# Kernel tuning notes

Measured on AMD Instinct MI355X. Metric: run time of the kernel, lower is better.

The kernel has to match this reference:

```python
import jax, jax.numpy as jnp
import numpy as np

EMBED_DIM = 512
NUM_HEADS = 8
HEAD_DIM = EMBED_DIM // NUM_HEADS


def setup_inputs() -> dict:
    key = jax.random.key(0)
    ks = jax.random.split(key, 9)
    s = 1.0 / np.sqrt(EMBED_DIM)
    x = jax.random.normal(ks[0], (2, 4096, EMBED_DIM), dtype=jnp.float32)
    return {
        "x": x,
        "Wq": jax.random.uniform(ks[1], (EMBED_DIM, EMBED_DIM), jnp.float32, -s, s),
        "bq": jax.random.uniform(ks[2], (EMBED_DIM,), jnp.float32, -s, s),
        "Wk": jax.random.uniform(ks[3], (EMBED_DIM, EMBED_DIM), jnp.float32, -s, s),
        "bk": jax.random.uniform(ks[4], (EMBED_DIM,), jnp.float32, -s, s),
        "Wv": jax.random.uniform(ks[5], (EMBED_DIM, EMBED_DIM), jnp.float32, -s, s),
        "bv": jax.random.uniform(ks[6], (EMBED_DIM,), jnp.float32, -s, s),
        "Wo": jax.random.uniform(ks[7], (EMBED_DIM, EMBED_DIM), jnp.float32, -s, s),
        "bo": jax.random.uniform(ks[8], (EMBED_DIM,), jnp.float32, -s, s),
    }


def reference(x, Wq, bq, Wk, bk, Wv, bv, Wo, bo):
    B, S, E = x.shape
    H, D = NUM_HEADS, HEAD_DIM
    # projections (torch Linear: x @ W.T + b)
    q = (x @ Wq.T + bq).reshape(B, S, H, D).transpose(0, 2, 1, 3)  # [B,H,S,D]
    k = (x @ Wk.T + bk).reshape(B, S, H, D).transpose(0, 2, 1, 3)
    v = (x @ Wv.T + bv).reshape(B, S, H, D).transpose(0, 2, 1, 3)
    scores = jnp.einsum("bhsd,bhtd->bhst", q, k) / np.sqrt(D)  # [B,H,S,S]
    attn = jax.nn.softmax(scores, axis=-1)
    out = jnp.einsum("bhst,bhtd->bhsd", attn, v)  # [B,H,S,D]
    out = out.transpose(0, 2, 1, 3).reshape(B, S, E)
    return out @ Wo.T + bo + x
```

## Files before the change

kernel.cpp:

```cpp
#include <hip/hip_runtime.h>
#include <hip/hip_bf16.h>


typedef __attribute__((ext_vector_type(8))) short short8;
typedef __attribute__((ext_vector_type(4))) float floatx4;

#define SEQ 4096
#define EMB 512
#define NH 8
#define HD 64
#define MROWS 8192
#define SC2 0.18033688011112042f

__device__ inline unsigned short f2bf_rne(float f) {
    union { float f; unsigned int u; } c; c.f = f;
    unsigned int u = c.u;
    return (unsigned short)((u + 0x7FFFu + ((u >> 16) & 1u)) >> 16);
}

__device__ inline short8 load8f(const float* __restrict__ p) {
    float4 a = *(const float4*)p;
    float4 b = *(const float4*)(p + 4);
    short8 r;
    r[0] = (short)f2bf_rne(a.x); r[1] = (short)f2bf_rne(a.y);
    r[2] = (short)f2bf_rne(a.z); r[3] = (short)f2bf_rne(a.w);
    r[4] = (short)f2bf_rne(b.x); r[5] = (short)f2bf_rne(b.y);
    r[6] = (short)f2bf_rne(b.z); r[7] = (short)f2bf_rne(b.w);
    return r;
}

__device__ inline void gload_lds16(const unsigned short* g, unsigned short* l) {
    __builtin_amdgcn_global_load_lds(
        (__attribute__((address_space(1))) void*)(void*)g,
        (__attribute__((address_space(3))) void*)l,
        16, 0, 0);
}

__global__ __launch_bounds__(256) void convert_kernel(
    const float* __restrict__ x, const float* __restrict__ Wq,
    const float* __restrict__ Wk, const float* __restrict__ Wv,
    const float* __restrict__ Wo, unsigned short* __restrict__ xb,
    unsigned short* __restrict__ wb)
{
    const size_t i8 = ((size_t)blockIdx.x * 256 + threadIdx.x) * 8;
    const float* src; unsigned short* dst;
    if (i8 < (size_t)MROWS * EMB) { src = x + i8; dst = xb + i8; }
    else {
        size_t j = i8 - (size_t)MROWS * EMB;
        int w = (int)(j >> 18); size_t off = j & 262143;
        src = (w == 0 ? Wq : w == 1 ? Wk : w == 2 ? Wv : Wo) + off;
        dst = wb + (size_t)w * 262144 + off;
    }
    *(short8*)dst = load8f(src);
}

__global__ __launch_bounds__(256) void qkv_kernel(
    const unsigned short* __restrict__ xb, const unsigned short* __restrict__ wb,
    const float* __restrict__ bq, const float* __restrict__ bk,
    const float* __restrict__ bv, unsigned short* __restrict__ Qo,
    unsigned short* __restrict__ Ko, unsigned short* __restrict__ VTo)
{
    __shared__ unsigned short sA[2][8192];
    __shared__ unsigned short sB[2][8192];

    const int tid = threadIdx.x, wave = tid >> 6, lane = tid & 63;
    const int quad = lane >> 4, l16 = lane & 15;
    const int wm = wave >> 1, wn = wave & 1;
    const int row0 = blockIdx.x * 128, col0 = blockIdx.y * 128;
    const int z = blockIdx.z;

    const unsigned short* A = xb + (size_t)row0 * EMB;
    const unsigned short* Bm = wb + (size_t)z * 262144 + (size_t)col0 * EMB;
    const float* bias = z == 0 ? bq : z == 1 ? bk : bv;
    unsigned short* out = z == 0 ? Qo : z == 1 ? Ko : VTo;

    auto stage = [&](int buf, int k0) {
#pragma unroll
        for (int it = 0; it < 4; ++it) {
            const int s = it * 256 + tid;
            const int row = s >> 3, cg = (s & 7) ^ (row & 7);
            const size_t go = (size_t)row * EMB + k0 + cg * 8;
            gload_lds16(A + go, &sA[buf][(it * 256 + wave * 64) * 8]);
            gload_lds16(Bm + go, &sB[buf][(it * 256 + wave * 64) * 8]);
        }
    };

    floatx4 acc[4][4];
#pragma unroll
    for (int mi = 0; mi < 4; ++mi)
#pragma unroll
        for (int ni = 0; ni < 4; ++ni) { floatx4 zz = {0.f,0.f,0.f,0.f}; acc[mi][ni] = zz; }

    stage(0, 0);
    int buf = 0;
    for (int k0 = 0; k0 < EMB; k0 += 64) {
        __syncthreads();
        if (k0 + 64 < EMB) stage(buf ^ 1, k0 + 64);
#pragma unroll
        for (int kk = 0; kk < 2; ++kk) {
            short8 a[4], b[4];
#pragma unroll
            for (int mi = 0; mi < 4; ++mi)
                a[mi] = *(const short8*)&sA[buf][(wm * 64 + mi * 16 + l16) * 64 + (((kk * 4 + quad) ^ (l16 & 7)) << 3)];
#pragma unroll
            for (int ni = 0; ni < 4; ++ni)
                b[ni] = *(const short8*)&sB[buf][(wn * 64 + ni * 16 + l16) * 64 + (((kk * 4 + quad) ^ (l16 & 7)) << 3)];
#pragma unroll
            for (int mi = 0; mi < 4; ++mi)
#pragma unroll
                for (int ni = 0; ni < 4; ++ni)
                    acc[mi][ni] = __builtin_amdgcn_mfma_f32_16x16x32_bf16(a[mi], b[ni], acc[mi][ni], 0, 0, 0);
        }
        buf ^= 1;
    }

    const float qs = (z == 0) ? SC2 : 1.0f;
#pragma unroll
    for (int mi = 0; mi < 4; ++mi)
#pragma unroll
        for (int ni = 0; ni < 4; ++ni) {
            const int n = col0 + wn * 64 + ni * 16 + l16;
            const float bs = bias[n];
            const int h = n >> 6, d = n & 63;
            if (z == 2) {
                const int m0 = row0 + wm * 64 + mi * 16 + quad * 4;
                const int b = m0 >> 12, s0 = m0 & 4095;
                ushort4 pk;
                pk.x = f2bf_rne(acc[mi][ni][0] + bs); pk.y = f2bf_rne(acc[mi][ni][1] + bs);
                pk.z = f2bf_rne(acc[mi][ni][2] + bs); pk.w = f2bf_rne(acc[mi][ni][3] + bs);
                *(ushort4*)&out[((size_t)((b * NH + h) * HD + d)) * SEQ + s0] = pk;
            } else {
#pragma unroll
                for (int r = 0; r < 4; ++r) {
                    const int m = row0 + wm * 64 + mi * 16 + quad * 4 + r;
                    const int b = m >> 12, s = m & 4095;
                    out[((size_t)((b * NH + h) * SEQ + s)) * HD + d] = f2bf_rne((acc[mi][ni][r] + bs) * qs);
                }
            }
        }
}

__global__ __launch_bounds__(256) void attn_kernel(
    const unsigned short* __restrict__ Q, const unsigned short* __restrict__ K,
    const unsigned short* __restrict__ VT, unsigned short* __restrict__ Oout)
{
    __shared__ unsigned short sK[2][4096];
    __shared__ unsigned short sVT[2][4096];
    __shared__ unsigned short sP[4][2048];

    const int tid = threadIdx.x, wave = tid >> 6, lane = tid & 63;
    const int quad = lane >> 4, l16 = lane & 15;
    const int bh = blockIdx.y, q0 = blockIdx.x * 128;

    const unsigned short* Qh = Q + (size_t)bh * SEQ * HD;
    const unsigned short* Kh = K + (size_t)bh * SEQ * HD;
    const unsigned short* Vh = VT + (size_t)bh * HD * SEQ;

    short8 qf[2][2];
#pragma unroll
    for (int mi = 0; mi < 2; ++mi)
#pragma unroll
        for (int kk = 0; kk < 2; ++kk)
            qf[mi][kk] = *(const short8*)(Qh + (size_t)(q0 + wave * 32 + mi * 16 + l16) * HD + kk * 32 + quad * 8);

    floatx4 oacc[2][4];
#pragma unroll
    for (int mi = 0; mi < 2; ++mi)
#pragma unroll
        for (int nt = 0; nt < 4; ++nt) { floatx4 zz = {0.f,0.f,0.f,0.f}; oacc[mi][nt] = zz; }
    float psum[2] = {0.f, 0.f};

    auto stage = [&](int buf, int t0) {
#pragma unroll
        for (int psi = 0; psi < 2; ++psi) {
            const int r = psi * 32 + wave * 8 + (lane >> 3);
            const int c = (lane & 7) ^ (r & 7);
            gload_lds16(Kh + (size_t)(t0 + r) * HD + c * 8, &sK[buf][psi * 2048 + wave * 512]);
            gload_lds16(Vh + (size_t)r * SEQ + t0 + c * 8, &sVT[buf][psi * 2048 + wave * 512]);
        }
    };

    stage(0, 0);
    int buf = 0;
    unsigned short* sPw = sP[wave];
    for (int t0 = 0; t0 < SEQ; t0 += 64) {
        __syncthreads();
        if (t0 + 64 < SEQ) stage(buf ^ 1, t0 + 64);

        floatx4 stf[2][4];
#pragma unroll
        for (int mi = 0; mi < 2; ++mi)
#pragma unroll
            for (int nt = 0; nt < 4; ++nt) { floatx4 zz = {0.f,0.f,0.f,0.f}; stf[mi][nt] = zz; }
#pragma unroll
        for (int kk = 0; kk < 2; ++kk) {
            short8 bK[4];
#pragma unroll
            for (int nt = 0; nt < 4; ++nt)
                bK[nt] = *(const short8*)&sK[buf][(nt * 16 + l16) * 64 + (((kk * 4 + quad) ^ (l16 & 7)) << 3)];
#pragma unroll
            for (int mi = 0; mi < 2; ++mi)
#pragma unroll
                for (int nt = 0; nt < 4; ++nt)
                    stf[mi][nt] = __builtin_amdgcn_mfma_f32_16x16x32_bf16(bK[nt], qf[mi][kk], stf[mi][nt], 0, 0, 0);
        }

#pragma unroll
        for (int mi = 0; mi < 2; ++mi) {
            const int q = mi * 16 + l16;
#pragma unroll
            for (int nt = 0; nt < 4; ++nt) {
                const float p0 = __builtin_amdgcn_exp2f(stf[mi][nt][0]);
                const float p1 = __builtin_amdgcn_exp2f(stf[mi][nt][1]);
                const float p2 = __builtin_amdgcn_exp2f(stf[mi][nt][2]);
                const float p3 = __builtin_amdgcn_exp2f(stf[mi][nt][3]);
                psum[mi] += (p0 + p1) + (p2 + p3);
                ushort4 pk;
                pk.x = f2bf_rne(p0); pk.y = f2bf_rne(p1);
                pk.z = f2bf_rne(p2); pk.w = f2bf_rne(p3);
                const int chunk = nt * 2 + (quad >> 1);
                *(ushort4*)&sPw[q * 64 + ((chunk ^ (q & 7)) << 3) + (quad & 1) * 4] = pk;
            }
        }

#pragma unroll
        for (int kk = 0; kk < 2; ++kk) {
            short8 bV[4], aP[2];
#pragma unroll
            for (int nt = 0; nt < 4; ++nt)
                bV[nt] = *(const short8*)&sVT[buf][(nt * 16 + l16) * 64 + (((kk * 4 + quad) ^ (l16 & 7)) << 3)];
#pragma unroll
            for (int mi = 0; mi < 2; ++mi)
                aP[mi] = *(const short8*)&sPw[(mi * 16 + l16) * 64 + (((kk * 4 + quad) ^ (l16 & 7)) << 3)];
#pragma unroll
            for (int mi = 0; mi < 2; ++mi)
#pragma unroll
                for (int nt = 0; nt < 4; ++nt)
                    oacc[mi][nt] = __builtin_amdgcn_mfma_f32_16x16x32_bf16(aP[mi], bV[nt], oacc[mi][nt], 0, 0, 0);
        }
        buf ^= 1;
    }

#pragma unroll
    for (int mi = 0; mi < 2; ++mi) {
        psum[mi] += __shfl_xor(psum[mi], 16);
        psum[mi] += __shfl_xor(psum[mi], 32);
    }

    const int b = bh >> 3, h = bh & 7;
#pragma unroll
    for (int mi = 0; mi < 2; ++mi)
#pragma unroll
        for (int r = 0; r < 4; ++r) {
            const float inv = 1.0f / __shfl(psum[mi], quad * 4 + r);
            const int s = q0 + wave * 32 + mi * 16 + quad * 4 + r;
            const size_t base = ((size_t)b * SEQ + s) * EMB + h * HD;
#pragma unroll
            for (int nt = 0; nt < 4; ++nt)
                Oout[base + nt * 16 + l16] = f2bf_rne(oacc[mi][nt][r] * inv);
        }
}

__global__ __launch_bounds__(256) void outproj_kernel(
    const unsigned short* __restrict__ Ain, const unsigned short* __restrict__ wob,
    const float* __restrict__ bias, const float* __restrict__ X,
    float* __restrict__ out)
{
    __shared__ unsigned short sA[2][4096];
    __shared__ unsigned short sB[2][8192];

    const int tid = threadIdx.x, wave = tid >> 6, lane = tid & 63;
    const int quad = lane >> 4, l16 = lane & 15;
    const int wm = wave >> 1, wn = wave & 1;
    const int row0 = blockIdx.x * 64, col0 = blockIdx.y * 128;

    const unsigned short* A = Ain + (size_t)row0 * EMB;
    const unsigned short* Bm = wob + (size_t)col0 * EMB;

    auto stage = [&](int buf, int k0) {
#pragma unroll
        for (int it = 0; it < 2; ++it) {
            const int s = it * 256 + tid;
            const int row = s >> 3, cg = (s & 7) ^ (row & 7);
            gload_lds16(A + (size_t)row * EMB + k0 + cg * 8, &sA[buf][(it * 256 + wave * 64) * 8]);
        }
#pragma unroll
        for (int it = 0; it < 4; ++it) {
            const int s = it * 256 + tid;
            const int row = s >> 3, cg = (s & 7) ^ (row & 7);
            gload_lds16(Bm + (size_t)row * EMB + k0 + cg * 8, &sB[buf][(it * 256 + wave * 64) * 8]);
        }
    };

    floatx4 acc[2][4];
#pragma unroll
    for (int mi = 0; mi < 2; ++mi)
#pragma unroll
        for (int ni = 0; ni < 4; ++ni) { floatx4 zz = {0.f,0.f,0.f,0.f}; acc[mi][ni] = zz; }

    stage(0, 0);
    int buf = 0;
    for (int k0 = 0; k0 < EMB; k0 += 64) {
        __syncthreads();
        if (k0 + 64 < EMB) stage(buf ^ 1, k0 + 64);
#pragma unroll
        for (int kk = 0; kk < 2; ++kk) {
            short8 a[2], b[4];
#pragma unroll
            for (int mi = 0; mi < 2; ++mi)
                a[mi] = *(const short8*)&sA[buf][(wm * 32 + mi * 16 + l16) * 64 + (((kk * 4 + quad) ^ (l16 & 7)) << 3)];
#pragma unroll
            for (int ni = 0; ni < 4; ++ni)
                b[ni] = *(const short8*)&sB[buf][(wn * 64 + ni * 16 + l16) * 64 + (((kk * 4 + quad) ^ (l16 & 7)) << 3)];
#pragma unroll
            for (int mi = 0; mi < 2; ++mi)
#pragma unroll
                for (int ni = 0; ni < 4; ++ni)
                    acc[mi][ni] = __builtin_amdgcn_mfma_f32_16x16x32_bf16(a[mi], b[ni], acc[mi][ni], 0, 0, 0);
        }
        buf ^= 1;
    }

#pragma unroll
    for (int mi = 0; mi < 2; ++mi)
#pragma unroll
        for (int ni = 0; ni < 4; ++ni) {
            const int n = col0 + wn * 64 + ni * 16 + l16;
            const float bs = bias[n];
#pragma unroll
            for (int r = 0; r < 4; ++r) {
                const int m = row0 + wm * 32 + mi * 16 + quad * 4 + r;
                const size_t idx = (size_t)m * EMB + n;
                out[idx] = acc[mi][ni][r] + bs + X[idx];
            }
        }
}

extern "C" void kernel_launch(void* const* d_in, const int* in_sizes, int n_in,
                              void* d_out, int out_size, void* d_ws, size_t ws_size,
                              hipStream_t stream) {
    const float* x  = (const float*)d_in[0];
    const float* Wq = (const float*)d_in[1];
    const float* bq = (const float*)d_in[2];
    const float* Wk = (const float*)d_in[3];
    const float* bk = (const float*)d_in[4];
    const float* Wv = (const float*)d_in[5];
    const float* bv = (const float*)d_in[6];
    const float* Wo = (const float*)d_in[7];
    const float* bo = (const float*)d_in[8];
    float* out = (float*)d_out;

    const size_t SZ = (size_t)MROWS * EMB;
    unsigned short* wsXB = (unsigned short*)d_ws;
    unsigned short* wsWB = wsXB + SZ;
    unsigned short* wsQ  = wsWB + 4 * 262144;
    unsigned short* wsK  = wsQ + SZ;
    unsigned short* wsVT = wsK + SZ;

    convert_kernel<<<2560, 256, 0, stream>>>(x, Wq, Wk, Wv, Wo, wsXB, wsWB);
    qkv_kernel<<<dim3(MROWS / 128, EMB / 128, 3), 256, 0, stream>>>(
        wsXB, wsWB, bq, bk, bv, wsQ, wsK, wsVT);
    attn_kernel<<<dim3(SEQ / 128, 2 * NH), 256, 0, stream>>>(wsQ, wsK, wsVT, wsXB);
    outproj_kernel<<<dim3(MROWS / 64, EMB / 128), 256, 0, stream>>>(
        wsXB, wsWB + 3 * 262144, bo, x, out);
}
```

Before: 225.1 us.

## Split attention KV range across two wave groups with LDS merge, store Q transposed

The attention kernel now runs 512 threads as two 4-wave groups. Each group processes alternating 64-key tiles of the same 128 queries, and the partial outputs and row sums are merged through LDS at the end. Double-buffered prefetch is replaced by a single-buffer load with two barriers per iteration. Q is written transposed by the QKV kernel, so the Q loads in attention become strided scalar gathers. P is packed to bf16 with a cheaper perm-based rounding (round-half-up rather than round-to-nearest-even), and the row sums are accumulated as float2 vectors. The aim is more waves per CU to hide latency, at the cost of losing load/compute overlap within each block.

Result: slower. 237.2 us (+5.4%).

```diff
diff --git a/kernel.cpp b/kernel.cpp
--- a/kernel.cpp
+++ b/kernel.cpp
@@ -4,6 +4,7 @@
 
 typedef __attribute__((ext_vector_type(8))) short short8;
 typedef __attribute__((ext_vector_type(4))) float floatx4;
+typedef __attribute__((ext_vector_type(2))) float floatx2;
 
 #define SEQ 4096
 #define EMB 512
@@ -34,6 +35,11 @@
         (__attribute__((address_space(1))) void*)(void*)g,
         (__attribute__((address_space(3))) void*)l,
         16, 0, 0);
+}
+
+__device__ inline unsigned int pk_bf2(float a, float b) {
+    union { float f; unsigned int u; } ca, cb; ca.f = a; cb.f = b;
+    return __builtin_amdgcn_perm(cb.u + 0x8000u, ca.u + 0x8000u, 0x07060302u);
 }
 
 __global__ __launch_bounds__(256) void convert_kernel(
@@ -57,7 +63,7 @@
 __global__ __launch_bounds__(256) void qkv_kernel(
     const unsigned short* __restrict__ xb, const unsigned short* __restrict__ wb,
     const float* __restrict__ bq, const float* __restrict__ bk,
-    const float* __restrict__ bv, unsigned short* __restrict__ Qo,
+    const float* __restrict__ bv, unsigned short* __restrict__ QTo,
     unsigned short* __restrict__ Ko, unsigned short* __restrict__ VTo)
 {
     __shared__ unsigned short sA[2][8192];
@@ -72,7 +78,7 @@
     const unsigned short* A = xb + (size_t)row0 * EMB;
     const unsigned short* Bm = wb + (size_t)z * 262144 + (size_t)col0 * EMB;
     const float* bias = z == 0 ? bq : z == 1 ? bk : bv;
-    unsigned short* out = z == 0 ? Qo : z == 1 ? Ko : VTo;
+    unsigned short* out = z == 0 ? QTo : z == 1 ? Ko : VTo;
 
     auto stage = [&](int buf, int k0) {
 #pragma unroll
@@ -122,70 +128,74 @@
             const int n = col0 + wn * 64 + ni * 16 + l16;
             const float bs = bias[n];
             const int h = n >> 6, d = n & 63;
-            if (z == 2) {
+            if (z != 1) {
                 const int m0 = row0 + wm * 64 + mi * 16 + quad * 4;
                 const int b = m0 >> 12, s0 = m0 & 4095;
                 ushort4 pk;
-                pk.x = f2bf_rne(acc[mi][ni][0] + bs); pk.y = f2bf_rne(acc[mi][ni][1] + bs);
-                pk.z = f2bf_rne(acc[mi][ni][2] + bs); pk.w = f2bf_rne(acc[mi][ni][3] + bs);
+                pk.x = f2bf_rne((acc[mi][ni][0] + bs) * qs);
+                pk.y = f2bf_rne((acc[mi][ni][1] + bs) * qs);
+                pk.z = f2bf_rne((acc[mi][ni][2] + bs) * qs);
+                pk.w = f2bf_rne((acc[mi][ni][3] + bs) * qs);
                 *(ushort4*)&out[((size_t)((b * NH + h) * HD + d)) * SEQ + s0] = pk;
             } else {
 #pragma unroll
                 for (int r = 0; r < 4; ++r) {
                     const int m = row0 + wm * 64 + mi * 16 + quad * 4 + r;
                     const int b = m >> 12, s = m & 4095;
-                    out[((size_t)((b * NH + h) * SEQ + s)) * HD + d] = f2bf_rne((acc[mi][ni][r] + bs) * qs);
+                    out[((size_t)((b * NH + h) * SEQ + s)) * HD + d] = f2bf_rne(acc[mi][ni][r] + bs);
                 }
             }
         }
 }
 
-__global__ __launch_bounds__(256) void attn_kernel(
-    const unsigned short* __restrict__ Q, const unsigned short* __restrict__ K,
+__global__ __launch_bounds__(512) void attn_kernel(
+    const unsigned short* __restrict__ QT, const unsigned short* __restrict__ K,
     const unsigned short* __restrict__ VT, unsigned short* __restrict__ Oout)
 {
-    __shared__ unsigned short sK[2][4096];
-    __shared__ unsigned short sVT[2][4096];
-    __shared__ unsigned short sP[4][2048];
+    __shared__ unsigned short smem[32768];
 
     const int tid = threadIdx.x, wave = tid >> 6, lane = tid & 63;
     const int quad = lane >> 4, l16 = lane & 15;
+    const int grp = wave >> 2, wl = wave & 3;
     const int bh = blockIdx.y, q0 = blockIdx.x * 128;
 
-    const unsigned short* Qh = Q + (size_t)bh * SEQ * HD;
-    const unsigned short* Kh = K + (size_t)bh * SEQ * HD;
-    const unsigned short* Vh = VT + (size_t)bh * HD * SEQ;
+    unsigned short* sKg  = smem + grp * 4096;
+    unsigned short* sVTg = smem + 8192 + grp * 4096;
+    unsigned short* sPw  = smem + 16384 + wave * 2048;
+
+    const unsigned short* QTh = QT + (size_t)bh * HD * SEQ;
+    const unsigned short* Kh  = K  + (size_t)bh * SEQ * HD;
+    const unsigned short* Vh  = VT + (size_t)bh * HD * SEQ;
 
     short8 qf[2][2];
 #pragma unroll
+    for (int mi = 0; mi < 2; ++mi) {
+        const int q = q0 + wl * 32 + mi * 16 + l16;
+#pragma unroll
+        for (int kk = 0; kk < 2; ++kk)
+#pragma unroll
+            for (int j = 0; j < 8; ++j)
+                qf[mi][kk][j] = (short)QTh[(size_t)(kk * 32 + quad * 8 + j) * SEQ + q];
+    }
+
+    floatx4 oacc[2][4];
+#pragma unroll
     for (int mi = 0; mi < 2; ++mi)
 #pragma unroll
-        for (int kk = 0; kk < 2; ++kk)
-            qf[mi][kk] = *(const short8*)(Qh + (size_t)(q0 + wave * 32 + mi * 16 + l16) * HD + kk * 32 + quad * 8);
-
-    floatx4 oacc[2][4];
-#pragma unroll
-    for (int mi = 0; mi < 2; ++mi)
-#pragma unroll
         for (int nt = 0; nt < 4; ++nt) { floatx4 zz = {0.f,0.f,0.f,0.f}; oacc[mi][nt] = zz; }
-    float psum[2] = {0.f, 0.f};
-
-    auto stage = [&](int buf, int t0) {
+    floatx2 psum2[2] = {{0.f, 0.f}, {0.f, 0.f}};
+
+    for (int it = 0; it < SEQ / 128; ++it) {
+        const int t0 = it * 128 + grp * 64;
+        __syncthreads();
 #pragma unroll
         for (int psi = 0; psi < 2; ++psi) {
-            const int r = psi * 32 + wave * 8 + (lane >> 3);
+            const int r = psi * 32 + wl * 8 + (lane >> 3);
             const int c = (lane & 7) ^ (r & 7);
-            gload_lds16(Kh + (size_t)(t0 + r) * HD + c * 8, &sK[buf][psi * 2048 + wave * 512]);
-            gload_lds16(Vh + (size_t)r * SEQ + t0 + c * 8, &sVT[buf][psi * 2048 + wave * 512]);
-        }
-    };
-
-    stage(0, 0);
-    int buf = 0;
-    unsigned short* sPw = sP[wave];
-    for (int t0 = 0; t0 < SEQ; t0 += 64) {
+            gload_lds16(Kh + (size_t)(t0 + r) * HD + c * 8, sKg + psi * 2048 + wl * 512);
+            gload_lds16(Vh + (size_t)r * SEQ + t0 + c * 8, sVTg + psi * 2048 + wl * 512);
+        }
         __syncthreads();
-        if (t0 + 64 < SEQ) stage(buf ^ 1, t0 + 64);
 
         floatx4 stf[2][4];
 #pragma unroll
@@ -197,7 +207,7 @@
             short8 bK[4];
 #pragma unroll
             for (int nt = 0; nt < 4; ++nt)
-                bK[nt] = *(const short8*)&sK[buf][(nt * 16 + l16) * 64 + (((kk * 4 + quad) ^ (l16 & 7)) << 3)];
+                bK[nt] = *(const short8*)&sKg[(nt * 16 + l16) * 64 + (((kk * 4 + quad) ^ (l16 & 7)) << 3)];
 #pragma unroll
             for (int mi = 0; mi < 2; ++mi)
 #pragma unroll
@@ -214,12 +224,13 @@
                 const float p1 = __builtin_amdgcn_exp2f(stf[mi][nt][1]);
                 const float p2 = __builtin_amdgcn_exp2f(stf[mi][nt][2]);
                 const float p3 = __builtin_amdgcn_exp2f(stf[mi][nt][3]);
-                psum[mi] += (p0 + p1) + (p2 + p3);
-                ushort4 pk;
-                pk.x = f2bf_rne(p0); pk.y = f2bf_rne(p1);
-                pk.z = f2bf_rne(p2); pk.w = f2bf_rne(p3);
+                floatx2 a = {p0, p1}, b = {p2, p3};
+                psum2[mi] += a + b;
+                uint2 pk;
+                pk.x = pk_bf2(p0, p1);
+                pk.y = pk_bf2(p2, p3);
                 const int chunk = nt * 2 + (quad >> 1);
-                *(ushort4*)&sPw[q * 64 + ((chunk ^ (q & 7)) << 3) + (quad & 1) * 4] = pk;
+                *(uint2*)&sPw[q * 64 + ((chunk ^ (q & 7)) << 3) + (quad & 1) * 4] = pk;
             }
         }
 
@@ -228,7 +239,7 @@
             short8 bV[4], aP[2];
 #pragma unroll
             for (int nt = 0; nt < 4; ++nt)
-                bV[nt] = *(const short8*)&sVT[buf][(nt * 16 + l16) * 64 + (((kk * 4 + quad) ^ (l16 & 7)) << 3)];
+                bV[nt] = *(const short8*)&sVTg[(nt * 16 + l16) * 64 + (((kk * 4 + quad) ^ (l16 & 7)) << 3)];
 #pragma unroll
             for (int mi = 0; mi < 2; ++mi)
                 aP[mi] = *(const short8*)&sPw[(mi * 16 + l16) * 64 + (((kk * 4 + quad) ^ (l16 & 7)) << 3)];
@@ -238,27 +249,46 @@
                 for (int nt = 0; nt < 4; ++nt)
                     oacc[mi][nt] = __builtin_amdgcn_mfma_f32_16x16x32_bf16(aP[mi], bV[nt], oacc[mi][nt], 0, 0, 0);
         }
-        buf ^= 1;
-    }
-
-#pragma unroll
-    for (int mi = 0; mi < 2; ++mi) {
-        psum[mi] += __shfl_xor(psum[mi], 16);
-        psum[mi] += __shfl_xor(psum[mi], 32);
-    }
-
-    const int b = bh >> 3, h = bh & 7;
-#pragma unroll
-    for (int mi = 0; mi < 2; ++mi)
-#pragma unroll
-        for (int r = 0; r < 4; ++r) {
-            const float inv = 1.0f / __shfl(psum[mi], quad * 4 + r);
-            const int s = q0 + wave * 32 + mi * 16 + quad * 4 + r;
-            const size_t base = ((size_t)b * SEQ + s) * EMB + h * HD;
+    }
+
+    float* mrg = (float*)smem;
+    __syncthreads();
+    if (grp == 1) {
+        float* p = mrg + wl * 2176 + lane * 34;
+#pragma unroll
+        for (int mi = 0; mi < 2; ++mi)
 #pragma unroll
             for (int nt = 0; nt < 4; ++nt)
-                Oout[base + nt * 16 + l16] = f2bf_rne(oacc[mi][nt][r] * inv);
-        }
+                *(floatx4*)(p + mi * 16 + nt * 4) = oacc[mi][nt];
+        p[32] = psum2[0][0] + psum2[0][1];
+        p[33] = psum2[1][0] + psum2[1][1];
+    }
+    __syncthreads();
+    if (grp == 0) {
+        const float* p = mrg + wl * 2176 + lane * 34;
+        float psum[2];
+#pragma unroll
+        for (int mi = 0; mi < 2; ++mi) {
+#pragma unroll
+            for (int nt = 0; nt < 4; ++nt)
+                oacc[mi][nt] += *(const floatx4*)(p + mi * 16 + nt * 4);
+            psum[mi] = psum2[mi][0] + psum2[mi][1] + p[32 + mi];
+            psum[mi] += __shfl_xor(psum[mi], 16);
+            psum[mi] += __shfl_xor(psum[mi], 32);
+        }
+        const int b = bh >> 3, h = bh & 7;
+#pragma unroll
+        for (int mi = 0; mi < 2; ++mi)
+#pragma unroll
+            for (int r = 0; r < 4; ++r) {
+                const float inv = 1.0f / __shfl(psum[mi], quad * 4 + r);
+                const int s = q0 + wl * 32 + mi * 16 + quad * 4 + r;
+                const size_t base = ((size_t)b * SEQ + s) * EMB + h * HD;
+#pragma unroll
+                for (int nt = 0; nt < 4; ++nt)
+                    Oout[base + nt * 16 + l16] = f2bf_rne(oacc[mi][nt][r] * inv);
+            }
+    }
 }
 
 __global__ __launch_bounds__(256) void outproj_kernel(
@@ -353,14 +383,14 @@
     const size_t SZ = (size_t)MROWS * EMB;
     unsigned short* wsXB = (unsigned short*)d_ws;
     unsigned short* wsWB = wsXB + SZ;
-    unsigned short* wsQ  = wsWB + 4 * 262144;
-    unsigned short* wsK  = wsQ + SZ;
+    unsigned short* wsQT = wsWB + 4 * 262144;
+    unsigned short* wsK  = wsQT + SZ;
     unsigned short* wsVT = wsK + SZ;
 
     convert_kernel<<<2560, 256, 0, stream>>>(x, Wq, Wk, Wv, Wo, wsXB, wsWB);
     qkv_kernel<<<dim3(MROWS / 128, EMB / 128, 3), 256, 0, stream>>>(
-        wsXB, wsWB, bq, bk, bv, wsQ, wsK, wsVT);
-    attn_kernel<<<dim3(SEQ / 128, 2 * NH), 256, 0, stream>>>(wsQ, wsK, wsVT, wsXB);
+        wsXB, wsWB, bq, bk, bv, wsQT, wsK, wsVT);
+    attn_kernel<<<dim3(SEQ / 128, 2 * NH), 512, 0, stream>>>(wsQT, wsK, wsVT, wsXB);
     outproj_kernel<<<dim3(MROWS / 64, EMB / 128), 256, 0, stream>>>(
         wsXB, wsWB + 3 * 262144, bo, x, out);
 }
```

## Stage QKV epilogue through LDS for coalesced stores; cheapen softmax bf16 packing

Applied to the files above, without the earlier changes.

The QKV projection epilogue now writes bias-added bf16 tiles into a padded LDS buffer that reuses the staging memory. It then issues 16-byte coalesced global stores for the Q/K and V-transposed layouts, replacing scattered 2-byte stores. For Q/K the MFMA operands are swapped so each lane holds four consecutive output columns, which allows a vectorized bias load. In the attention kernel, P is converted to bf16 with a perm-based round-half-up pack instead of full round-to-nearest-even, and the row sum uses packed float2 adds. This slightly changes rounding on ties.

Result: faster. 217.1 us (-3.6%).

```diff
diff --git a/kernel.cpp b/kernel.cpp
--- a/kernel.cpp
+++ b/kernel.cpp
@@ -4,6 +4,7 @@
 
 typedef __attribute__((ext_vector_type(8))) short short8;
 typedef __attribute__((ext_vector_type(4))) float floatx4;
+typedef __attribute__((ext_vector_type(2))) float floatx2;
 
 #define SEQ 4096
 #define EMB 512
@@ -34,6 +35,11 @@
         (__attribute__((address_space(1))) void*)(void*)g,
         (__attribute__((address_space(3))) void*)l,
         16, 0, 0);
+}
+
+__device__ inline unsigned int pk_bf2(float a, float b) {
+    union { float f; unsigned int u; } ca, cb; ca.f = a; cb.f = b;
+    return __builtin_amdgcn_perm(cb.u + 0x8000u, ca.u + 0x8000u, 0x07060302u);
 }
 
 __global__ __launch_bounds__(256) void convert_kernel(
@@ -60,8 +66,7 @@
     const float* __restrict__ bv, unsigned short* __restrict__ Qo,
     unsigned short* __restrict__ Ko, unsigned short* __restrict__ VTo)
 {
-    __shared__ unsigned short sA[2][8192];
-    __shared__ unsigned short sB[2][8192];
+    __shared__ unsigned short smem[32768];
 
     const int tid = threadIdx.x, wave = tid >> 6, lane = tid & 63;
     const int quad = lane >> 4, l16 = lane & 15;
@@ -69,6 +74,9 @@
     const int row0 = blockIdx.x * 128, col0 = blockIdx.y * 128;
     const int z = blockIdx.z;
 
+    unsigned short* sA = smem;
+    unsigned short* sB = smem + 16384;
+
     const unsigned short* A = xb + (size_t)row0 * EMB;
     const unsigned short* Bm = wb + (size_t)z * 262144 + (size_t)col0 * EMB;
     const float* bias = z == 0 ? bq : z == 1 ? bk : bv;
@@ -80,16 +88,16 @@
             const int s = it * 256 + tid;
             const int row = s >> 3, cg = (s & 7) ^ (row & 7);
             const size_t go = (size_t)row * EMB + k0 + cg * 8;
-            gload_lds16(A + go, &sA[buf][(it * 256 + wave * 64) * 8]);
-            gload_lds16(Bm + go, &sB[buf][(it * 256 + wave * 64) * 8]);
+            gload_lds16(A + go, &sA[buf * 8192 + (it * 256 + wave * 64) * 8]);
+            gload_lds16(Bm + go, &sB[buf * 8192 + (it * 256 + wave * 64) * 8]);
         }
     };
 
     floatx4 acc[4][4];
 #pragma unroll
-    for (int mi = 0; mi < 4; ++mi)
-#pragma unroll
-        for (int ni = 0; ni < 4; ++ni) { floatx4 zz = {0.f,0.f,0.f,0.f}; acc[mi][ni] = zz; }
+    for (int i = 0; i < 4; ++i)
+#pragma unroll
+        for (int j = 0; j < 4; ++j) { floatx4 zz = {0.f,0.f,0.f,0.f}; acc[i][j] = zz; }
 
     stage(0, 0);
     int buf = 0;
@@ -101,43 +109,85 @@
             short8 a[4], b[4];
 #pragma unroll
             for (int mi = 0; mi < 4; ++mi)
-                a[mi] = *(const short8*)&sA[buf][(wm * 64 + mi * 16 + l16) * 64 + (((kk * 4 + quad) ^ (l16 & 7)) << 3)];
+                a[mi] = *(const short8*)&sA[buf * 8192 + (wm * 64 + mi * 16 + l16) * 64 + (((kk * 4 + quad) ^ (l16 & 7)) << 3)];
 #pragma unroll
             for (int ni = 0; ni < 4; ++ni)
-                b[ni] = *(const short8*)&sB[buf][(wn * 64 + ni * 16 + l16) * 64 + (((kk * 4 + quad) ^ (l16 & 7)) << 3)];
-#pragma unroll
-            for (int mi = 0; mi < 4; ++mi)
-#pragma unroll
-                for (int ni = 0; ni < 4; ++ni)
-                    acc[mi][ni] = __builtin_amdgcn_mfma_f32_16x16x32_bf16(a[mi], b[ni], acc[mi][ni], 0, 0, 0);
+                b[ni] = *(const short8*)&sB[buf * 8192 + (wn * 64 + ni * 16 + l16) * 64 + (((kk * 4 + quad) ^ (l16 & 7)) << 3)];
+            if (z != 2) {
+#pragma unroll
+                for (int i = 0; i < 4; ++i)
+#pragma unroll
+                    for (int j = 0; j < 4; ++j)
+                        acc[i][j] = __builtin_amdgcn_mfma_f32_16x16x32_bf16(b[i], a[j], acc[i][j], 0, 0, 0);
+            } else {
+#pragma unroll
+                for (int i = 0; i < 4; ++i)
+#pragma unroll
+                    for (int j = 0; j < 4; ++j)
+                        acc[i][j] = __builtin_amdgcn_mfma_f32_16x16x32_bf16(a[i], b[j], acc[i][j], 0, 0, 0);
+            }
         }
         buf ^= 1;
     }
 
+    __syncthreads();
+    unsigned short* ct = smem;
     const float qs = (z == 0) ? SC2 : 1.0f;
-#pragma unroll
-    for (int mi = 0; mi < 4; ++mi)
-#pragma unroll
-        for (int ni = 0; ni < 4; ++ni) {
-            const int n = col0 + wn * 64 + ni * 16 + l16;
-            const float bs = bias[n];
-            const int h = n >> 6, d = n & 63;
-            if (z == 2) {
-                const int m0 = row0 + wm * 64 + mi * 16 + quad * 4;
-                const int b = m0 >> 12, s0 = m0 & 4095;
+    if (z != 2) {
+#pragma unroll
+        for (int i = 0; i < 4; ++i) {
+            const int n0 = wn * 64 + i * 16 + quad * 4;
+            const float4 fb = *(const float4*)&bias[col0 + n0];
+#pragma unroll
+            for (int j = 0; j < 4; ++j) {
+                const int m = wm * 64 + j * 16 + l16;
                 ushort4 pk;
-                pk.x = f2bf_rne(acc[mi][ni][0] + bs); pk.y = f2bf_rne(acc[mi][ni][1] + bs);
-                pk.z = f2bf_rne(acc[mi][ni][2] + bs); pk.w = f2bf_rne(acc[mi][ni][3] + bs);
-                *(ushort4*)&out[((size_t)((b * NH + h) * HD + d)) * SEQ + s0] = pk;
-            } else {
-#pragma unroll
-                for (int r = 0; r < 4; ++r) {
-                    const int m = row0 + wm * 64 + mi * 16 + quad * 4 + r;
-                    const int b = m >> 12, s = m & 4095;
-                    out[((size_t)((b * NH + h) * SEQ + s)) * HD + d] = f2bf_rne((acc[mi][ni][r] + bs) * qs);
-                }
+                pk.x = f2bf_rne((acc[i][j][0] + fb.x) * qs);
+                pk.y = f2bf_rne((acc[i][j][1] + fb.y) * qs);
+                pk.z = f2bf_rne((acc[i][j][2] + fb.z) * qs);
+                pk.w = f2bf_rne((acc[i][j][3] + fb.w) * qs);
+                *(ushort4*)&ct[m * 132 + n0] = pk;
             }
         }
+    } else {
+#pragma unroll
+        for (int j = 0; j < 4; ++j) {
+            const int n = wn * 64 + j * 16 + l16;
+            const float fb = bias[col0 + n];
+#pragma unroll
+            for (int i = 0; i < 4; ++i) {
+                const int m0 = wm * 64 + i * 16 + quad * 4;
+                ushort4 pk;
+                pk.x = f2bf_rne(acc[i][j][0] + fb);
+                pk.y = f2bf_rne(acc[i][j][1] + fb);
+                pk.z = f2bf_rne(acc[i][j][2] + fb);
+                pk.w = f2bf_rne(acc[i][j][3] + fb);
+                *(ushort4*)&ct[n * 132 + m0] = pk;
+            }
+        }
+    }
+    __syncthreads();
+#pragma unroll
+    for (int it = 0; it < 8; ++it) {
+        const int idx = it * 256 + tid;
+        const int row = idx >> 4, chunk = idx & 15;
+        short8 v = *(const short8*)&ct[row * 132 + chunk * 8];
+        size_t addr;
+        if (z != 2) {
+            const int m_g = row0 + row;
+            const int b = m_g >> 12, s = m_g & 4095;
+            const int n_g = col0 + chunk * 8;
+            const int h = n_g >> 6, d = n_g & 63;
+            addr = ((size_t)((b * NH + h) * SEQ + s)) * HD + d;
+        } else {
+            const int n_g = col0 + row;
+            const int h = n_g >> 6, d = n_g & 63;
+            const int m_g = row0 + chunk * 8;
+            const int b = m_g >> 12, s0 = m_g & 4095;
+            addr = ((size_t)((b * NH + h) * HD + d)) * SEQ + s0;
+        }
+        *(short8*)&out[addr] = v;
+    }
 }
 
 __global__ __launch_bounds__(256) void attn_kernel(
@@ -168,7 +218,7 @@
     for (int mi = 0; mi < 2; ++mi)
 #pragma unroll
         for (int nt = 0; nt < 4; ++nt) { floatx4 zz = {0.f,0.f,0.f,0.f}; oacc[mi][nt] = zz; }
-    float psum[2] = {0.f, 0.f};
+    floatx2 psum2[2] = {{0.f, 0.f}, {0.f, 0.f}};
 
     auto stage = [&](int buf, int t0) {
 #pragma unroll
@@ -214,12 +264,13 @@
                 const float p1 = __builtin_amdgcn_exp2f(stf[mi][nt][1]);
                 const float p2 = __builtin_amdgcn_exp2f(stf[mi][nt][2]);
                 const float p3 = __builtin_amdgcn_exp2f(stf[mi][nt][3]);
-                psum[mi] += (p0 + p1) + (p2 + p3);
-                ushort4 pk;
-                pk.x = f2bf_rne(p0); pk.y = f2bf_rne(p1);
-                pk.z = f2bf_rne(p2); pk.w = f2bf_rne(p3);
+                floatx2 a = {p0, p1}, b = {p2, p3};
+                psum2[mi] += a + b;
+                uint2 pk;
+                pk.x = pk_bf2(p0, p1);
+                pk.y = pk_bf2(p2, p3);
                 const int chunk = nt * 2 + (quad >> 1);
-                *(ushort4*)&sPw[q * 64 + ((chunk ^ (q & 7)) << 3) + (quad & 1) * 4] = pk;
+                *(uint2*)&sPw[q * 64 + ((chunk ^ (q & 7)) << 3) + (quad & 1) * 4] = pk;
             }
         }
 
@@ -241,8 +292,10 @@
         buf ^= 1;
     }
 
+    float psum[2];
 #pragma unroll
     for (int mi = 0; mi < 2; ++mi) {
+        psum[mi] = psum2[mi][0] + psum2[mi][1];
         psum[mi] += __shfl_xor(psum[mi], 16);
         psum[mi] += __shfl_xor(psum[mi], 32);
     }
```
